# Kernel optimization log

Hardware: AMD Instinct MI355X
Metric: run time of the kernel (lower is better)

## Reference

```python
import jax, jax.numpy as jnp
import numpy as np

K, B, C, T, D, H = 4, 1024, 128, 64, 64, 4  # timeframes, batch, in-feat, seq(=embed!), embed, heads
HD = D // H
EPS = 1e-5


def setup_inputs() -> dict:
    key = jax.random.key(0)
    ks = jax.random.split(key, 8)
    s = lambda k, shape: jax.random.normal(k, shape, dtype=jnp.float32) * 0.05
    return {
        "feats": jax.random.normal(ks[0], (K, B, C, T), dtype=jnp.float32),
        "proj_w": s(ks[1], (K, D, C)),
        "proj_b": jnp.zeros((K, D), jnp.float32),
        "wq": s(ks[2], (K, D, D)),
        "wk": s(ks[3], (K, D, D)),
        "wv": s(ks[4], (K, D, D)),
        "bq": jnp.zeros((K, D), jnp.float32),
        "bk": jnp.zeros((K, D), jnp.float32),
        "bv": jnp.zeros((K, D), jnp.float32),
        "wo": s(ks[5], (K, D, D)),
        "bo": jnp.zeros((K, D), jnp.float32),
        "ng": jnp.ones((K, D), jnp.float32),
        "nb": jnp.zeros((K, D), jnp.float32),
        "tfw": jnp.full((K,), 1.0 / K, jnp.float32),
        "fg": jnp.ones((K * D,), jnp.float32),
        "fb": jnp.zeros((K * D,), jnp.float32),
    }


def _ln(x, g, b):
    m = x.mean(-1, keepdims=True)
    v = ((x - m) ** 2).mean(-1, keepdims=True)
    return (x - m) * jax.lax.rsqrt(v + EPS) * g + b


def reference(feats, proj_w, proj_b, wq, wk, wv, bq, bk, bv, wo, bo, ng, nb, tfw, fg, fb):
    # per-timeframe Linear on channel axis: [K,B,C,T] -> [K,B,D,T]
    proj = jnp.einsum('kbct,kdc->kbdt', feats, proj_w) + proj_b[:, None, :, None]
    ctx4 = jnp.transpose(proj, (1, 0, 2, 3))              # [B,K,D,T] (torch.stack dim=1)
    ctx = ctx4.reshape(B * D, K, T)                       # replicates torch .view(B*T,K,D); needs T==D
    N = B * D
    scale = 1.0 / np.sqrt(HD)
    outs = []
    for i in range(K):  # small fixed loop over K=4 distinct attention blocks
        q_in = ctx[:, i]                                  # [N,D] query = i-th row
        q = (q_in @ wq[i].T + bq[i]).reshape(N, H, HD)
        k = (ctx @ wk[i].T + bk[i]).reshape(N, K, H, HD)
        v = (ctx @ wv[i].T + bv[i]).reshape(N, K, H, HD)
        sc = jnp.einsum('nhe,nkhe->nhk', q, k) * scale    # [N,H,K]
        a = jax.nn.softmax(sc, axis=-1)
        o = jnp.einsum('nhk,nkhe->nhe', a, v).reshape(N, D)
        o = o @ wo[i].T + bo[i]
        outs.append(_ln(o + q_in, ng[i], nb[i]))          # residual + per-tf LayerNorm
    w = jax.nn.softmax(tfw)
    comb = jnp.stack(outs, axis=1) * w[None, :, None]     # [N,K,D] weighted fusion
    fused = comb.reshape(B, D, K * D)                     # torch .view(B,T,K*D)
    return _ln(fused, fg, fb)
```

## Files before the change

### kernel.cpp

```cpp
#include <hip/hip_runtime.h>
#include <math.h>

#define EPSV 1e-5f

typedef __attribute__((ext_vector_type(8))) short short8;
typedef __attribute__((ext_vector_type(4))) float float4v;
typedef __attribute__((ext_vector_type(4))) unsigned short ushort4v;

__device__ __forceinline__ unsigned short f2bf(float f) {
  unsigned int x = __float_as_uint(f);
  return (unsigned short)((x + 0x7fffu + ((x >> 16) & 1u)) >> 16);
}
__device__ __forceinline__ float bf2f(unsigned short u) {
  return __uint_as_float(((unsigned int)u) << 16);
}
__device__ __forceinline__ float wave_sum64(float v) {
  v += __shfl_xor(v, 1);
  v += __shfl_xor(v, 2);
  v += __shfl_xor(v, 4);
  v += __shfl_xor(v, 8);
  v += __shfl_xor(v, 16);
  v += __shfl_xor(v, 32);
  return v;
}
__device__ __forceinline__ float group16_sum(float v) {
  v += __shfl_xor(v, 1);
  v += __shfl_xor(v, 2);
  v += __shfl_xor(v, 4);
  v += __shfl_xor(v, 8);
  return v;
}
__device__ __forceinline__ void lds_fence() {
  asm volatile("s_waitcnt lgkmcnt(0)" ::: "memory");
}

__global__ __launch_bounds__(256) void prep_kernel(
    const float* __restrict__ pw, const float* __restrict__ wq,
    const float* __restrict__ wk, const float* __restrict__ wv,
    const float* __restrict__ wo, unsigned short* __restrict__ wph,
    unsigned short* __restrict__ wpl, unsigned short* __restrict__ wb) {
  int idx = blockIdx.x * 256 + threadIdx.x;
  if (idx < 32768) {
    float f = pw[idx];
    unsigned short h = f2bf(f);
    wph[idx] = h;
    wpl[idx] = f2bf(f - bf2f(h));
  } else {
    int e = idx - 32768;
    int mat = e >> 14, i = (e >> 12) & 3, r = e & 4095;
    const float* src = (mat == 0) ? wq : (mat == 1) ? wk : (mat == 2) ? wv : wo;
    wb[((i * 4 + mat) << 12) + r] = f2bf(src[(i << 12) + r]);
  }
}

__global__ __launch_bounds__(256, 4) void proj_kernel(
    const float* __restrict__ feats, const unsigned short* __restrict__ wph,
    const unsigned short* __restrict__ wpl, const float* __restrict__ pb,
    unsigned short* __restrict__ ctxbf) {
  int kb = blockIdx.x;
  int k = kb >> 10;
  int b = kb & 1023;

  __shared__ __align__(16) unsigned short FH[64 * 128];
  __shared__ __align__(16) unsigned short FL[64 * 128];

  int tid = threadIdx.x;
  const float* fsrc = feats + (size_t)kb * 8192;
#pragma unroll
  for (int it = 0; it < 4; ++it) {
    int e = it * 256 + tid;
    int t = e & 63;
    int cg = e >> 6;
    float fv[8];
#pragma unroll
    for (int q = 0; q < 8; ++q) fv[q] = fsrc[(cg * 8 + q) * 64 + t];
    short8 hv, lv;
#pragma unroll
    for (int q = 0; q < 8; ++q) {
      unsigned short h = f2bf(fv[q]);
      hv[q] = (short)h;
      lv[q] = (short)f2bf(fv[q] - bf2f(h));
    }
    int u = cg ^ (t & 15);
    *(short8*)&FH[t * 128 + u * 8] = hv;
    *(short8*)&FL[t * 128 + u * 8] = lv;
  }
  __syncthreads();

  int w = tid >> 6, l = tid & 63;
  int l15 = l & 15, lq = l >> 4;

  const float4v zf = {0.0f, 0.0f, 0.0f, 0.0f};
  float4v acc[4] = {zf, zf, zf, zf};

  const unsigned short* whp = wph + k * 8192 + (w * 16 + l15) * 128 + lq * 8;
  const unsigned short* wlp = wpl + k * 8192 + (w * 16 + l15) * 128 + lq * 8;

  __builtin_amdgcn_s_setprio(1);
#pragma unroll
  for (int kc = 0; kc < 4; ++kc) {
    short8 ah = *(const short8*)&whp[kc * 32];
    short8 al = *(const short8*)&wlp[kc * 32];
#pragma unroll
    for (int nt = 0; nt < 4; ++nt) {
      int boff = (nt * 16 + l15) * 128 + (((kc * 4 + lq) ^ l15) * 8);
      short8 bh = *(const short8*)&FH[boff];
      short8 bl = *(const short8*)&FL[boff];
      acc[nt] = __builtin_amdgcn_mfma_f32_16x16x32_bf16(ah, bh, acc[nt], 0, 0, 0);
      acc[nt] = __builtin_amdgcn_mfma_f32_16x16x32_bf16(ah, bl, acc[nt], 0, 0, 0);
      acc[nt] = __builtin_amdgcn_mfma_f32_16x16x32_bf16(al, bh, acc[nt], 0, 0, 0);
    }
  }
  __builtin_amdgcn_s_setprio(0);

  float pbv[4];
#pragma unroll
  for (int r = 0; r < 4; ++r) pbv[r] = pb[k * 64 + w * 16 + lq * 4 + r];

  size_t base = ((size_t)b * 64 + k * 16 + w * 4 + lq) * 256;
#pragma unroll
  for (int nt = 0; nt < 4; ++nt)
#pragma unroll
    for (int r = 0; r < 4; ++r)
      ctxbf[base + r * 64 + nt * 16 + l15] = f2bf(acc[nt][r] + pbv[r]);
}

__global__ __launch_bounds__(256, 2) void attn_fused(
    const unsigned short* __restrict__ ctxbf,
    const unsigned short* __restrict__ wb,
    const float* __restrict__ bq, const float* __restrict__ bk,
    const float* __restrict__ bv, const float* __restrict__ bo,
    const float* __restrict__ ng, const float* __restrict__ nb,
    const float* __restrict__ tfw, const float* __restrict__ fg,
    const float* __restrict__ fb, float* __restrict__ out) {
  __shared__ __align__(16) unsigned short CTP[64 * 264];
  __shared__ __align__(16) unsigned short OSP[4][16 * 72];
  __shared__ __align__(16) unsigned short CMB[64 * 256];

  int tid = threadIdx.x;
  int w = tid >> 6, l = tid & 63;
  int l15 = l & 15, lq = l >> 4;

  {
    const unsigned short* csrc = ctxbf + ((size_t)blockIdx.x * 64 + w * 16) * 256;
#pragma unroll
    for (int u = 0; u < 8; ++u) {
      int e = u * 64 + l;
      int row = e >> 5, c8 = (e & 31) * 8;
      *(short8*)&CTP[(w * 16 + row) * 264 + c8] =
          *(const short8*)&csrc[row * 256 + c8];
    }
  }
  lds_fence();

  float tf0 = tfw[0], tf1 = tfw[1], tf2 = tfw[2], tf3 = tfw[3];
  float tm = fmaxf(fmaxf(tf0, tf1), fmaxf(tf2, tf3));
  float te0 = __expf(tf0 - tm), te1 = __expf(tf1 - tm);
  float te2 = __expf(tf2 - tm), te3 = __expf(tf3 - tm);
  float tden = te0 + te1 + te2 + te3;

  const unsigned short* arow = &CTP[(w * 16 + l15) * 264];
  const float4v zf = {0.0f, 0.0f, 0.0f, 0.0f};

#pragma unroll 1
  for (int i = 0; i < 4; ++i) {
#define WFRAG(m, nt, s)                                                        \
  (*(const short8*)&wb[((i * 4 + (m)) << 12) + ((nt)*16 + l15) * 64 +          \
                       (s)*32 + lq * 8])

    float wi = ((i == 0) ? te0 : (i == 1) ? te1 : (i == 2) ? te2 : te3) / tden;

    float bqv[4], bkv[4], bvv[4];
#pragma unroll
    for (int nt = 0; nt < 4; ++nt) {
      int d = i * 64 + nt * 16 + l15;
      bqv[nt] = bq[d]; bkv[nt] = bk[d]; bvv[nt] = bv[d];
    }

    float4v qacc[4] = {zf, zf, zf, zf};
    __builtin_amdgcn_s_setprio(1);
#pragma unroll
    for (int s = 0; s < 2; ++s) {
      short8 af = *(const short8*)&arow[i * 64 + s * 32 + lq * 8];
#pragma unroll
      for (int nt = 0; nt < 4; ++nt)
        qacc[nt] = __builtin_amdgcn_mfma_f32_16x16x32_bf16(af, WFRAG(0, nt, s),
                                                           qacc[nt], 0, 0, 0);
    }
    __builtin_amdgcn_s_setprio(0);
#pragma unroll
    for (int nt = 0; nt < 4; ++nt)
#pragma unroll
      for (int r = 0; r < 4; ++r) qacc[nt][r] += bqv[nt];

    short8 kf[2][4], vf[2][4];
#pragma unroll
    for (int s = 0; s < 2; ++s)
#pragma unroll
      for (int nt = 0; nt < 4; ++nt) {
        kf[s][nt] = WFRAG(1, nt, s);
        vf[s][nt] = WFRAG(2, nt, s);
      }

    float4v oacc[4] = {zf, zf, zf, zf};
    float lsum[4][4] = {{0,0,0,0},{0,0,0,0},{0,0,0,0},{0,0,0,0}};

#pragma unroll 1
    for (int j = 0; j < 4; ++j) {
      float4v kacc[4] = {zf, zf, zf, zf};
      float4v vacc[4] = {zf, zf, zf, zf};
      __builtin_amdgcn_s_setprio(1);
#pragma unroll
      for (int s = 0; s < 2; ++s) {
        short8 af = *(const short8*)&arow[j * 64 + s * 32 + lq * 8];
#pragma unroll
        for (int nt = 0; nt < 4; ++nt) {
          kacc[nt] = __builtin_amdgcn_mfma_f32_16x16x32_bf16(af, kf[s][nt],
                                                             kacc[nt], 0, 0, 0);
          vacc[nt] = __builtin_amdgcn_mfma_f32_16x16x32_bf16(af, vf[s][nt],
                                                             vacc[nt], 0, 0, 0);
        }
      }
      __builtin_amdgcn_s_setprio(0);
#pragma unroll
      for (int nt = 0; nt < 4; ++nt)
#pragma unroll
        for (int r = 0; r < 4; ++r) {
          float p = qacc[nt][r] * (kacc[nt][r] + bkv[nt]);
          p = group16_sum(p) * 0.25f;
          float e = __expf(p);
          lsum[nt][r] += e;
          oacc[nt][r] += e * (vacc[nt][r] + bvv[nt]);
        }
    }

    lds_fence();
#pragma unroll
    for (int nt = 0; nt < 4; ++nt)
#pragma unroll
      for (int r = 0; r < 4; ++r)
        OSP[w][(lq * 4 + r) * 72 + nt * 16 + l15] = f2bf(oacc[nt][r] / lsum[nt][r]);
    lds_fence();

    float4v o2[4] = {zf, zf, zf, zf};
    __builtin_amdgcn_s_setprio(1);
#pragma unroll
    for (int s = 0; s < 2; ++s) {
      short8 af = *(const short8*)&OSP[w][l15 * 72 + s * 32 + lq * 8];
#pragma unroll
      for (int nt = 0; nt < 4; ++nt)
        o2[nt] = __builtin_amdgcn_mfma_f32_16x16x32_bf16(af, WFRAG(3, nt, s),
                                                         o2[nt], 0, 0, 0);
    }
    __builtin_amdgcn_s_setprio(0);

    float bov[4], ngv[4], nbv[4];
#pragma unroll
    for (int nt = 0; nt < 4; ++nt) {
      int d = i * 64 + nt * 16 + l15;
      bov[nt] = bo[d]; ngv[nt] = ng[d]; nbv[nt] = nb[d];
    }

    float rr[4][4];
#pragma unroll
    for (int nt = 0; nt < 4; ++nt)
#pragma unroll
      for (int r = 0; r < 4; ++r) {
        float qin = bf2f(CTP[(w * 16 + lq * 4 + r) * 264 + i * 64 + nt * 16 + l15]);
        rr[nt][r] = o2[nt][r] + bov[nt] + qin;
      }

#pragma unroll
    for (int r = 0; r < 4; ++r) {
      float sm = group16_sum(rr[0][r] + rr[1][r] + rr[2][r] + rr[3][r]) * (1.0f / 64.0f);
      float vs = 0.0f;
#pragma unroll
      for (int nt = 0; nt < 4; ++nt) { float dx = rr[nt][r] - sm; vs += dx * dx; }
      vs = group16_sum(vs) * (1.0f / 64.0f);
      float inv = rsqrtf(vs + EPSV);
      int rowl = w * 16 + lq * 4 + r;
#pragma unroll
      for (int nt = 0; nt < 4; ++nt) {
        float val = wi * ((rr[nt][r] - sm) * inv * ngv[nt] + nbv[nt]);
        CMB[rowl * 256 + i * 64 + nt * 16 + l15] = f2bf(val);
      }
    }
#undef WFRAG
  }

  lds_fence();
  float4 g = *(const float4*)&fg[l * 4];
  float4 bb = *(const float4*)&fb[l * 4];
#pragma unroll 1
  for (int rr = 0; rr < 16; ++rr) {
    int rowl = w * 16 + rr;
    ushort4v pk = *(const ushort4v*)&CMB[rowl * 256 + l * 4];
    float vx = bf2f(pk.x), vy = bf2f(pk.y), vz = bf2f(pk.z), vw = bf2f(pk.w);
    float mean = wave_sum64(vx + vy + vz + vw) * (1.0f / 256.0f);
    float dx = vx - mean, dy = vy - mean, dz = vz - mean, dw = vw - mean;
    float var = wave_sum64(dx * dx + dy * dy + dz * dz + dw * dw) * (1.0f / 256.0f);
    float inv = rsqrtf(var + EPSV);
    float4 o;
    o.x = dx * inv * g.x + bb.x;
    o.y = dy * inv * g.y + bb.y;
    o.z = dz * inv * g.z + bb.z;
    o.w = dw * inv * g.w + bb.w;
    *(float4*)&out[((size_t)blockIdx.x * 64 + rowl) * 256 + l * 4] = o;
  }
}

extern "C" void kernel_launch(void* const* d_in, const int* in_sizes, int n_in,
                              void* d_out, int out_size, void* d_ws, size_t ws_size,
                              hipStream_t stream) {
  const float* feats  = (const float*)d_in[0];
  const float* proj_w = (const float*)d_in[1];
  const float* proj_b = (const float*)d_in[2];
  const float* wq  = (const float*)d_in[3];
  const float* wk  = (const float*)d_in[4];
  const float* wv  = (const float*)d_in[5];
  const float* bq  = (const float*)d_in[6];
  const float* bk  = (const float*)d_in[7];
  const float* bv  = (const float*)d_in[8];
  const float* wo  = (const float*)d_in[9];
  const float* bo  = (const float*)d_in[10];
  const float* ng  = (const float*)d_in[11];
  const float* nb  = (const float*)d_in[12];
  const float* tfw = (const float*)d_in[13];
  const float* fg  = (const float*)d_in[14];
  const float* fb  = (const float*)d_in[15];
  float* out = (float*)d_out;

  unsigned short* ctxbf = (unsigned short*)d_ws;
  unsigned short* wph = (unsigned short*)((char*)d_ws + ((size_t)32 << 20));
  unsigned short* wpl = wph + 32768;
  unsigned short* wb  = wpl + 32768;

  prep_kernel<<<384, 256, 0, stream>>>(proj_w, wq, wk, wv, wo, wph, wpl, wb);
  proj_kernel<<<4096, 256, 0, stream>>>(feats, wph, wpl, proj_b, ctxbf);
  attn_fused<<<1024, 256, 0, stream>>>(ctxbf, wb, bq, bk, bv, bo,
                                       ng, nb, tfw, fg, fb, out);
}
```

Before: 354.3 us.

## Fuse projection into attention kernel, keep ctx in LDS instead of global

```diff
diff --git a/kernel.cpp b/kernel.cpp
--- a/kernel.cpp
+++ b/kernel.cpp
@@ -53,105 +53,84 @@
   }
 }
 
-__global__ __launch_bounds__(256, 4) void proj_kernel(
+__global__ __launch_bounds__(256, 2) void fused_kernel(
     const float* __restrict__ feats, const unsigned short* __restrict__ wph,
     const unsigned short* __restrict__ wpl, const float* __restrict__ pb,
-    unsigned short* __restrict__ ctxbf) {
-  int kb = blockIdx.x;
-  int k = kb >> 10;
-  int b = kb & 1023;
-
-  __shared__ __align__(16) unsigned short FH[64 * 128];
-  __shared__ __align__(16) unsigned short FL[64 * 128];
-
-  int tid = threadIdx.x;
-  const float* fsrc = feats + (size_t)kb * 8192;
-#pragma unroll
-  for (int it = 0; it < 4; ++it) {
-    int e = it * 256 + tid;
-    int t = e & 63;
-    int cg = e >> 6;
-    float fv[8];
-#pragma unroll
-    for (int q = 0; q < 8; ++q) fv[q] = fsrc[(cg * 8 + q) * 64 + t];
-    short8 hv, lv;
-#pragma unroll
-    for (int q = 0; q < 8; ++q) {
-      unsigned short h = f2bf(fv[q]);
-      hv[q] = (short)h;
-      lv[q] = (short)f2bf(fv[q] - bf2f(h));
-    }
-    int u = cg ^ (t & 15);
-    *(short8*)&FH[t * 128 + u * 8] = hv;
-    *(short8*)&FL[t * 128 + u * 8] = lv;
-  }
-  __syncthreads();
-
-  int w = tid >> 6, l = tid & 63;
-  int l15 = l & 15, lq = l >> 4;
-
-  const float4v zf = {0.0f, 0.0f, 0.0f, 0.0f};
-  float4v acc[4] = {zf, zf, zf, zf};
-
-  const unsigned short* whp = wph + k * 8192 + (w * 16 + l15) * 128 + lq * 8;
-  const unsigned short* wlp = wpl + k * 8192 + (w * 16 + l15) * 128 + lq * 8;
-
-  __builtin_amdgcn_s_setprio(1);
-#pragma unroll
-  for (int kc = 0; kc < 4; ++kc) {
-    short8 ah = *(const short8*)&whp[kc * 32];
-    short8 al = *(const short8*)&wlp[kc * 32];
-#pragma unroll
-    for (int nt = 0; nt < 4; ++nt) {
-      int boff = (nt * 16 + l15) * 128 + (((kc * 4 + lq) ^ l15) * 8);
-      short8 bh = *(const short8*)&FH[boff];
-      short8 bl = *(const short8*)&FL[boff];
-      acc[nt] = __builtin_amdgcn_mfma_f32_16x16x32_bf16(ah, bh, acc[nt], 0, 0, 0);
-      acc[nt] = __builtin_amdgcn_mfma_f32_16x16x32_bf16(ah, bl, acc[nt], 0, 0, 0);
-      acc[nt] = __builtin_amdgcn_mfma_f32_16x16x32_bf16(al, bh, acc[nt], 0, 0, 0);
-    }
-  }
-  __builtin_amdgcn_s_setprio(0);
-
-  float pbv[4];
-#pragma unroll
-  for (int r = 0; r < 4; ++r) pbv[r] = pb[k * 64 + w * 16 + lq * 4 + r];
-
-  size_t base = ((size_t)b * 64 + k * 16 + w * 4 + lq) * 256;
-#pragma unroll
-  for (int nt = 0; nt < 4; ++nt)
-#pragma unroll
-    for (int r = 0; r < 4; ++r)
-      ctxbf[base + r * 64 + nt * 16 + l15] = f2bf(acc[nt][r] + pbv[r]);
-}
-
-__global__ __launch_bounds__(256, 2) void attn_fused(
-    const unsigned short* __restrict__ ctxbf,
     const unsigned short* __restrict__ wb,
     const float* __restrict__ bq, const float* __restrict__ bk,
     const float* __restrict__ bv, const float* __restrict__ bo,
     const float* __restrict__ ng, const float* __restrict__ nb,
     const float* __restrict__ tfw, const float* __restrict__ fg,
     const float* __restrict__ fb, float* __restrict__ out) {
+  __shared__ __align__(16) unsigned short POOL[2 * 64 * 136];
   __shared__ __align__(16) unsigned short CTP[64 * 264];
   __shared__ __align__(16) unsigned short OSP[4][16 * 72];
-  __shared__ __align__(16) unsigned short CMB[64 * 256];
+
+  unsigned short* const FH = POOL;
+  unsigned short* const FL = POOL + 64 * 136;
+  unsigned short* const CMB = POOL;
 
   int tid = threadIdx.x;
   int w = tid >> 6, l = tid & 63;
   int l15 = l & 15, lq = l >> 4;
-
-  {
-    const unsigned short* csrc = ctxbf + ((size_t)blockIdx.x * 64 + w * 16) * 256;
-#pragma unroll
-    for (int u = 0; u < 8; ++u) {
-      int e = u * 64 + l;
-      int row = e >> 5, c8 = (e & 31) * 8;
-      *(short8*)&CTP[(w * 16 + row) * 264 + c8] =
-          *(const short8*)&csrc[row * 256 + c8];
-    }
+  const float4v zf = {0.0f, 0.0f, 0.0f, 0.0f};
+
+#pragma unroll 1
+  for (int k = 0; k < 4; ++k) {
+    __syncthreads();
+    const float* fsrc = feats + ((size_t)k * 1024 + blockIdx.x) * 8192;
+#pragma unroll
+    for (int it = 0; it < 4; ++it) {
+      int e = it * 256 + tid;
+      int t = e & 63;
+      int cg = e >> 6;
+      float fv[8];
+#pragma unroll
+      for (int q = 0; q < 8; ++q) fv[q] = fsrc[(cg * 8 + q) * 64 + t];
+      short8 hv, lv;
+#pragma unroll
+      for (int q = 0; q < 8; ++q) {
+        unsigned short h = f2bf(fv[q]);
+        hv[q] = (short)h;
+        lv[q] = (short)f2bf(fv[q] - bf2f(h));
+      }
+      *(short8*)&FH[t * 136 + cg * 8] = hv;
+      *(short8*)&FL[t * 136 + cg * 8] = lv;
+    }
+    __syncthreads();
+
+    float4v acc[4] = {zf, zf, zf, zf};
+    const unsigned short* whp = wph + k * 8192 + (w * 16 + l15) * 128 + lq * 8;
+    const unsigned short* wlp = wpl + k * 8192 + (w * 16 + l15) * 128 + lq * 8;
+
+    __builtin_amdgcn_s_setprio(1);
+#pragma unroll
+    for (int kc = 0; kc < 4; ++kc) {
+      short8 ah = *(const short8*)&whp[kc * 32];
+      short8 al = *(const short8*)&wlp[kc * 32];
+#pragma unroll
+      for (int nt = 0; nt < 4; ++nt) {
+        short8 bh = *(const short8*)&FH[(nt * 16 + l15) * 136 + kc * 32 + lq * 8];
+        short8 bl = *(const short8*)&FL[(nt * 16 + l15) * 136 + kc * 32 + lq * 8];
+        acc[nt] = __builtin_amdgcn_mfma_f32_16x16x32_bf16(ah, bh, acc[nt], 0, 0, 0);
+        acc[nt] = __builtin_amdgcn_mfma_f32_16x16x32_bf16(ah, bl, acc[nt], 0, 0, 0);
+        acc[nt] = __builtin_amdgcn_mfma_f32_16x16x32_bf16(al, bh, acc[nt], 0, 0, 0);
+      }
+    }
+    __builtin_amdgcn_s_setprio(0);
+
+    float pbv[4];
+#pragma unroll
+    for (int r = 0; r < 4; ++r) pbv[r] = pb[k * 64 + w * 16 + lq * 4 + r];
+
+#pragma unroll
+    for (int nt = 0; nt < 4; ++nt)
+#pragma unroll
+      for (int r = 0; r < 4; ++r)
+        CTP[(k * 16 + w * 4 + lq) * 264 + r * 64 + nt * 16 + l15] =
+            f2bf(acc[nt][r] + pbv[r]);
   }
-  lds_fence();
+  __syncthreads();
 
   float tf0 = tfw[0], tf1 = tfw[1], tf2 = tfw[2], tf3 = tfw[3];
   float tm = fmaxf(fmaxf(tf0, tf1), fmaxf(tf2, tf3));
@@ -160,7 +139,6 @@
   float tden = te0 + te1 + te2 + te3;
 
   const unsigned short* arow = &CTP[(w * 16 + l15) * 264];
-  const float4v zf = {0.0f, 0.0f, 0.0f, 0.0f};
 
 #pragma unroll 1
   for (int i = 0; i < 4; ++i) {
@@ -330,13 +308,12 @@
   const float* fb  = (const float*)d_in[15];
   float* out = (float*)d_out;
 
-  unsigned short* ctxbf = (unsigned short*)d_ws;
-  unsigned short* wph = (unsigned short*)((char*)d_ws + ((size_t)32 << 20));
+  unsigned short* wph = (unsigned short*)d_ws;
   unsigned short* wpl = wph + 32768;
   unsigned short* wb  = wpl + 32768;
 
   prep_kernel<<<384, 256, 0, stream>>>(proj_w, wq, wk, wv, wo, wph, wpl, wb);
-  proj_kernel<<<4096, 256, 0, stream>>>(feats, wph, wpl, proj_b, ctxbf);
-  attn_fused<<<1024, 256, 0, stream>>>(ctxbf, wb, bq, bk, bv, bo,
-                                       ng, nb, tfw, fg, fb, out);
-}
+  fused_kernel<<<1024, 256, 0, stream>>>(feats, wph, wpl, proj_b, wb,
+                                         bq, bk, bv, bo, ng, nb, tfw,
+                                         fg, fb, out);
+}
```

Result: faster. 343.5 us (-3.0%).
